# Performance work log

Hardware: AMD Instinct MI355X
Metric: run time of the kernel (lower is better)

## Reference

```python
import jax, jax.numpy as jnp
import numpy as np

N_Q = 9      # qubits -> state dim 512
N_L = 10     # circuit layers
DIM = 2 ** N_Q
B = 16384    # batch
N_CLS = 10


def _apply_1q(psi, U, q):
    # psi: [B, 2,...,2] (N_Q qubit axes); U: [2,2] complex
    psi = jnp.moveaxis(psi, q + 1, 1)
    shp = psi.shape
    psi = jnp.einsum('ij,bjk->bik', U, psi.reshape(shp[0], 2, -1)).reshape(shp)
    return jnp.moveaxis(psi, 1, q + 1)


def _apply_2q(psi, U, q0, q1):
    # U: [4,4] complex acting on (q0, q1)
    psi = jnp.moveaxis(psi, (q0 + 1, q1 + 1), (1, 2))
    shp = psi.shape
    psi = jnp.einsum('ij,bjk->bik', U, psi.reshape(shp[0], 4, -1)).reshape(shp)
    return jnp.moveaxis(psi, (1, 2), (q0 + 1, q1 + 1))


def _rot_mat(phi, theta, omega):
    # PennyLane Rot = RZ(omega) RY(theta) RZ(phi)
    c, s = jnp.cos(theta / 2), jnp.sin(theta / 2)
    a, b = (phi + omega) / 2, (phi - omega) / 2
    return jnp.stack([
        jnp.stack([jnp.exp(-1j * a) * c, -jnp.exp(1j * b) * s]),
        jnp.stack([jnp.exp(-1j * b) * s, jnp.exp(1j * a) * c]),
    ]).astype(jnp.complex64)


def _crx_mat(t):
    c, s = jnp.cos(t / 2), jnp.sin(t / 2)
    rx = jnp.stack([jnp.stack([c + 0j, -1j * s]),
                    jnp.stack([-1j * s, c + 0j])]).astype(jnp.complex64)
    return jnp.eye(4, dtype=jnp.complex64).at[2:, 2:].set(rx)


def _layer(psi, rot_n, crx_n):
    for i in range(N_Q):
        psi = _apply_1q(psi, _rot_mat(rot_n[i, 0], rot_n[i, 1], rot_n[i, 2]), i)
    for i in range(N_Q):
        psi = _apply_2q(psi, _crx_mat(crx_n[i, 0]), i, (i + 1) % N_Q)
    return psi


def _circuit(x, rot, crx):
    # AmplitudeEmbedding(normalize=True)
    psi = (x / jnp.linalg.norm(x, axis=1, keepdims=True)).astype(jnp.complex64)
    psi = psi.reshape((x.shape[0],) + (2,) * N_Q)
    for n in range(N_L):
        psi = _layer(psi, rot[n], crx[n])
    probs = psi.real ** 2 + psi.imag ** 2
    # <Z_q> = P(bit_q = 0) - P(bit_q = 1)
    zs = []
    for q in range(N_Q):
        axes = tuple(a for a in range(1, N_Q + 1) if a != q + 1)
        p = probs.sum(axis=axes)  # [B, 2]
        zs.append(p[:, 0] - p[:, 1])
    return jnp.stack(zs, axis=1)  # [B, N_Q]


def setup_inputs() -> dict:
    key = jax.random.key(0)
    k0, k1, k2, k3, k4 = jax.random.split(key, 5)
    x = jax.random.normal(k0, (B, DIM), jnp.float32)
    rot = jax.random.normal(k1, (N_L, N_Q, 3), jnp.float32)
    crx = jax.random.normal(k2, (N_L, N_Q, 1), jnp.float32)
    fc_w = jax.random.normal(k3, (N_CLS, N_Q), jnp.float32) * 0.3
    fc_b = jax.random.normal(k4, (N_CLS,), jnp.float32) * 0.1
    return {"x": x, "rot": rot, "crx": crx, "fc_w": fc_w, "fc_b": fc_b}


def reference(x, rot, crx, fc_w, fc_b):
    z = _circuit(x, rot, crx)          # [B, 9]
    logits = z @ fc_w.T + fc_b         # [B, 10]
    return jax.nn.log_softmax(logits, axis=1)
```

## Files before the change

kernel.cpp:

```cpp
#include <hip/hip_runtime.h>
#include <hip/hip_bf16.h>
#include <math.h>

#define NQ 9
#define NL 10
#define DIM 512
#define NCLS 10
#define B_TOT 16384

#define A_OFF   ((size_t)0)
#define BT_OFF  ((size_t)16 << 20)
#define ZP_OFF  ((size_t)32 << 20)
#define WS_NEED (((size_t)96) << 20)

__device__ __forceinline__ float shx(float v, int m) { return __shfl_xor(v, m, 64); }

__device__ __forceinline__ int looks_bf16(const void* p, int count) {
  const unsigned short* u = (const unsigned short*)p;
  int n = count < 64 ? count : 64;
  int good = 0;
  for (int i = 0; i < n; ++i) {
    unsigned short v = u[i];
    int e = (v >> 7) & 0xFF;
    good += (e >= 100 && e <= 140) || ((v & 0x7FFF) == 0);
  }
  return good * 8 >= n * 7;
}

__device__ __forceinline__ float ld(const void* p, int i, int isbf) {
  if (isbf) return __uint_as_float(((unsigned)((const unsigned short*)p)[i]) << 16);
  return ((const float*)p)[i];
}

template<int M>
__device__ __forceinline__ void rot_x(float (&sr)[8], float (&si)[8], const float* u) {
  float4 uA = *(const float4*)u;
  float4 uB = *(const float4*)(u + 4);
  bool hi = (threadIdx.x & M) != 0;
  float ar = hi ? uB.z : uA.x, ai = hi ? uB.w : uA.y;
  float br = hi ? uB.x : uA.z, bi = hi ? uB.y : uA.w;
#pragma unroll
  for (int r = 0; r < 8; ++r) {
    float pr = shx(sr[r], M), pi = shx(si[r], M);
    float nr = ar * sr[r] - ai * si[r] + br * pr - bi * pi;
    float ni = ar * si[r] + ai * sr[r] + br * pi + bi * pr;
    sr[r] = nr; si[r] = ni;
  }
}
template<int S>
__device__ __forceinline__ void rot_r(float (&sr)[8], float (&si)[8], const float* u) {
  float4 uA = *(const float4*)u;
  float4 uB = *(const float4*)(u + 4);
#pragma unroll
  for (int r0 = 0; r0 < 8; ++r0) {
    if (r0 & S) continue;
    int r1 = r0 + S;
    float a0r = sr[r0], a0i = si[r0], a1r = sr[r1], a1i = si[r1];
    sr[r0] = uA.x * a0r - uA.y * a0i + uA.z * a1r - uA.w * a1i;
    si[r0] = uA.x * a0i + uA.y * a0r + uA.z * a1i + uA.w * a1r;
    sr[r1] = uB.x * a0r - uB.y * a0i + uB.z * a1r - uB.w * a1i;
    si[r1] = uB.x * a0i + uB.y * a0r + uB.z * a1i + uB.w * a1r;
  }
}
template<int MC, int MT>
__device__ __forceinline__ void crx_ll(float (&sr)[8], float (&si)[8], const float* cs) {
  bool ctrl = (threadIdx.x & MC) != 0;
  float c = ctrl ? cs[0] : 1.0f;
  float s = ctrl ? cs[1] : 0.0f;
#pragma unroll
  for (int r = 0; r < 8; ++r) {
    float pr = shx(sr[r], MT), pi = shx(si[r], MT);
    float nr = c * sr[r] + s * pi;
    float ni = c * si[r] - s * pr;
    sr[r] = nr; si[r] = ni;
  }
}
template<int MC, int ST>
__device__ __forceinline__ void crx_lr(float (&sr)[8], float (&si)[8], const float* cs) {
  bool ctrl = (threadIdx.x & MC) != 0;
  float c = ctrl ? cs[0] : 1.0f;
  float s = ctrl ? cs[1] : 0.0f;
#pragma unroll
  for (int r0 = 0; r0 < 8; ++r0) {
    if (r0 & ST) continue;
    int r1 = r0 + ST;
    float a0r = sr[r0], a0i = si[r0], a1r = sr[r1], a1i = si[r1];
    sr[r0] = c * a0r + s * a1i;  si[r0] = c * a0i - s * a1r;
    sr[r1] = c * a1r + s * a0i;  si[r1] = c * a1i - s * a0r;
  }
}
template<int PC, int ST>
__device__ __forceinline__ void crx_rr(float (&sr)[8], float (&si)[8], const float* cs) {
  float c = cs[0], s = cs[1];
#pragma unroll
  for (int r0 = 0; r0 < 8; ++r0) {
    if (r0 & ST) continue;
    if (!((r0 >> PC) & 1)) continue;
    int r1 = r0 + ST;
    float a0r = sr[r0], a0i = si[r0], a1r = sr[r1], a1i = si[r1];
    sr[r0] = c * a0r + s * a1i;  si[r0] = c * a0i - s * a1r;
    sr[r1] = c * a1r + s * a0i;  si[r1] = c * a1i - s * a0r;
  }
}
template<int PC, int MT>
__device__ __forceinline__ void crx_rl(float (&sr)[8], float (&si)[8], const float* cs) {
  float c = cs[0], s = cs[1];
#pragma unroll
  for (int r = 0; r < 8; ++r) {
    if (!((r >> PC) & 1)) continue;
    float pr = shx(sr[r], MT), pi = shx(si[r], MT);
    float nr = c * sr[r] + s * pi;
    float ni = c * si[r] - s * pr;
    sr[r] = nr; si[r] = ni;
  }
}

__device__ __forceinline__ void build_gates(const void* rot, const void* crx,
                                            float* gU, float* gCS) {
  int tid = threadIdx.x;
  __shared__ int gflags[2];
  if (tid == 0) {
    gflags[0] = looks_bf16(rot, NL * NQ * 3);
    gflags[1] = looks_bf16(crx, NL * NQ);
  }
  __syncthreads();
  if (tid < NL * NQ) {
    int frot = gflags[0], fcrx = gflags[1];
    float phi = ld(rot, tid * 3 + 0, frot);
    float th  = ld(rot, tid * 3 + 1, frot);
    float om  = ld(rot, tid * 3 + 2, frot);
    float c = cosf(0.5f * th), s = sinf(0.5f * th);
    float a = 0.5f * (phi + om), b = 0.5f * (phi - om);
    float ca = cosf(a), sa = sinf(a), cb = cosf(b), sb = sinf(b);
    float* u = gU + tid * 8;
    u[0] =  ca * c; u[1] = -sa * c;
    u[2] = -cb * s; u[3] = -sb * s;
    u[4] =  cb * s; u[5] = -sb * s;
    u[6] =  ca * c; u[7] =  sa * c;
    float t2 = 0.5f * ld(crx, tid, fcrx);
    gCS[tid * 2 + 0] = cosf(t2);
    gCS[tid * 2 + 1] = sinf(t2);
  }
  __syncthreads();
}

__device__ __forceinline__ void run_circuit(float (&sr)[8], float (&si)[8],
                                            const float* gU, const float* gCS) {
#pragma unroll 1
  for (int n = 0; n < NL; ++n) {
    const float* U  = gU  + n * NQ * 8;
    const float* CS = gCS + n * NQ * 2;
    rot_x<32>(sr, si, U + 0 * 8);
    rot_x<16>(sr, si, U + 1 * 8);
    rot_x< 8>(sr, si, U + 2 * 8);
    rot_x< 4>(sr, si, U + 3 * 8);
    rot_x< 2>(sr, si, U + 4 * 8);
    rot_x< 1>(sr, si, U + 5 * 8);
    rot_r< 4>(sr, si, U + 6 * 8);
    rot_r< 2>(sr, si, U + 7 * 8);
    rot_r< 1>(sr, si, U + 8 * 8);
    crx_ll<32, 16>(sr, si, CS + 0 * 2);
    crx_ll<16,  8>(sr, si, CS + 1 * 2);
    crx_ll< 8,  4>(sr, si, CS + 2 * 2);
    crx_ll< 4,  2>(sr, si, CS + 3 * 2);
    crx_ll< 2,  1>(sr, si, CS + 4 * 2);
    crx_lr< 1,  4>(sr, si, CS + 5 * 2);
    crx_rr< 2,  2>(sr, si, CS + 6 * 2);
    crx_rr< 1,  1>(sr, si, CS + 7 * 2);
    crx_rl< 0, 32>(sr, si, CS + 8 * 2);
  }
}

template<int M>
__device__ __forceinline__ void rot_lane2(float (&sr)[2], float (&si)[2], const float* u) {
  float4 uA = *(const float4*)u;
  float4 uB = *(const float4*)(u + 4);
  bool hi = (threadIdx.x & M) != 0;
  float ar = hi ? uB.z : uA.x, ai = hi ? uB.w : uA.y;
  float br = hi ? uB.x : uA.z, bi = hi ? uB.y : uA.w;
#pragma unroll
  for (int r = 0; r < 2; ++r) {
    float pr = shx(sr[r], M), pi = shx(si[r], M);
    float nr = ar * sr[r] - ai * si[r] + br * pr - bi * pi;
    float ni = ar * si[r] + ai * sr[r] + br * pi + bi * pr;
    sr[r] = nr; si[r] = ni;
  }
}
__device__ __forceinline__ void rot_reg2(float (&sr)[2], float (&si)[2], const float* u) {
  float4 uA = *(const float4*)u;
  float4 uB = *(const float4*)(u + 4);
  float a0r = sr[0], a0i = si[0], a1r = sr[1], a1i = si[1];
  sr[0] = uA.x * a0r - uA.y * a0i + uA.z * a1r - uA.w * a1i;
  si[0] = uA.x * a0i + uA.y * a0r + uA.z * a1i + uA.w * a1r;
  sr[1] = uB.x * a0r - uB.y * a0i + uB.z * a1r - uB.w * a1i;
  si[1] = uB.x * a0i + uB.y * a0r + uB.z * a1i + uB.w * a1r;
}
__device__ __forceinline__ void crx_lane2(float (&sr)[2], float (&si)[2],
                                          float c, float s, int MT) {
#pragma unroll
  for (int r = 0; r < 2; ++r) {
    float pr = shx(sr[r], MT), pi = shx(si[r], MT);
    float nr = c * sr[r] + s * pi;
    float ni = c * si[r] - s * pr;
    sr[r] = nr; si[r] = ni;
  }
}
__device__ __forceinline__ void crx_reg2(float (&sr)[2], float (&si)[2], float c, float s) {
  float a0r = sr[0], a0i = si[0], a1r = sr[1], a1i = si[1];
  sr[0] = c * a0r + s * a1i;  si[0] = c * a0i - s * a1r;
  sr[1] = c * a1r + s * a0i;  si[1] = c * a1i - s * a0r;
}

__global__ __launch_bounds__(256) void prep_kernel(const void* __restrict__ x,
                                                   const void* __restrict__ rot,
                                                   const void* __restrict__ crx,
                                                   __hip_bfloat16* __restrict__ A,
                                                   __hip_bfloat16* __restrict__ BT) {
  int tid = threadIdx.x;
  if (blockIdx.x < DIM) {
    __shared__ __align__(16) float gU[NL * NQ * 8];
    __shared__ __align__(16) float gCS[NL * NQ * 2];
    __shared__ float sRe[DIM], sIm[DIM];
    build_gates(rot, crx, gU, gCS);
    int lane = tid & 63, wv = tid >> 6;
    int idx0 = wv * 128 + lane * 2;
    int k = blockIdx.x;
    float sr[2], si[2];
    sr[0] = (idx0 == k) ? 1.f : 0.f;
    sr[1] = (idx0 + 1 == k) ? 1.f : 0.f;
    si[0] = si[1] = 0.f;
#pragma unroll 1
    for (int n = 0; n < NL; ++n) {
      const float* U   = gU  + n * NQ * 8;
      const float* CS  = gCS + n * NQ * 2;
      const float* CSp = gCS + (n - 1) * NQ * 2;
      __syncthreads();
      sRe[idx0] = sr[0]; sIm[idx0] = si[0];
      sRe[idx0 + 1] = sr[1]; sIm[idx0 + 1] = si[1];
      __syncthreads();
      {
        const float* U0 = U; const float* U1 = U + 8;
        int a = wv >> 1, b = wv & 1;
        float mr[4], mi[4];
#pragma unroll
        for (int w2 = 0; w2 < 4; ++w2) {
          int a2 = w2 >> 1, b2 = w2 & 1;
          float u0r = U0[(a * 2 + a2) * 2], u0i = U0[(a * 2 + a2) * 2 + 1];
          float u1r = U1[(b * 2 + b2) * 2], u1i = U1[(b * 2 + b2) * 2 + 1];
          mr[w2] = u0r * u1r - u0i * u1i;
          mi[w2] = u0r * u1i + u0i * u1r;
        }
        float x0r[4], x0i[4], v1r[4], v1i[4];
#pragma unroll
        for (int w2 = 0; w2 < 4; ++w2) {
          x0r[w2] = sRe[w2 * 128 + lane * 2 + 0];
          x0i[w2] = sIm[w2 * 128 + lane * 2 + 0];
          v1r[w2] = sRe[w2 * 128 + lane * 2 + 1];
          v1i[w2] = sIm[w2 * 128 + lane * 2 + 1];
        }
        float x1r[4], x1i[4];
        if (n > 0) {
          float cp = CSp[16], sp = CSp[17];
#pragma unroll
          for (int w2 = 0; w2 < 4; ++w2) {
            x1r[w2] = cp * v1r[w2] + sp * v1i[w2 ^ 2];
            x1i[w2] = cp * v1i[w2] - sp * v1r[w2 ^ 2];
          }
        } else {
#pragma unroll
          for (int w2 = 0; w2 < 4; ++w2) { x1r[w2] = v1r[w2]; x1i[w2] = v1i[w2]; }
        }
        float nr0 = 0.f, ni0 = 0.f, nr1 = 0.f, ni1 = 0.f;
#pragma unroll
        for (int w2 = 0; w2 < 4; ++w2) {
          nr0 += mr[w2] * x0r[w2] - mi[w2] * x0i[w2];
          ni0 += mr[w2] * x0i[w2] + mi[w2] * x0r[w2];
          nr1 += mr[w2] * x1r[w2] - mi[w2] * x1i[w2];
          ni1 += mr[w2] * x1i[w2] + mi[w2] * x1r[w2];
        }
        sr[0] = nr0; si[0] = ni0; sr[1] = nr1; si[1] = ni1;
      }
      rot_lane2<32>(sr, si, U + 2 * 8);
      rot_lane2<16>(sr, si, U + 3 * 8);
      rot_lane2< 8>(sr, si, U + 4 * 8);
      rot_lane2< 4>(sr, si, U + 5 * 8);
      rot_lane2< 2>(sr, si, U + 6 * 8);
      rot_lane2< 1>(sr, si, U + 7 * 8);
      rot_reg2(sr, si, U + 8 * 8);
      __syncthreads();
      sRe[idx0] = sr[0]; sIm[idx0] = si[0];
      sRe[idx0 + 1] = sr[1]; sIm[idx0 + 1] = si[1];
      __syncthreads();
      {
        float c = (wv & 2) ? CS[0] : 1.f, s = (wv & 2) ? CS[1] : 0.f;
        int p0 = (wv ^ 1) * 128 + lane * 2;
#pragma unroll
        for (int r = 0; r < 2; ++r) {
          float pr = sRe[p0 + r], pi = sIm[p0 + r];
          float nr = c * sr[r] + s * pi;
          float ni = c * si[r] - s * pr;
          sr[r] = nr; si[r] = ni;
        }
      }
      { float c = (wv & 1) ? CS[2] : 1.f, s = (wv & 1) ? CS[3] : 0.f;
        crx_lane2(sr, si, c, s, 32); }
      { bool ct = (lane & 32); crx_lane2(sr, si, ct ? CS[4] : 1.f, ct ? CS[5] : 0.f, 16); }
      { bool ct = (lane & 16); crx_lane2(sr, si, ct ? CS[6] : 1.f, ct ? CS[7] : 0.f, 8); }
      { bool ct = (lane &  8); crx_lane2(sr, si, ct ? CS[8] : 1.f, ct ? CS[9] : 0.f, 4); }
      { bool ct = (lane &  4); crx_lane2(sr, si, ct ? CS[10] : 1.f, ct ? CS[11] : 0.f, 2); }
      { bool ct = (lane &  2); crx_lane2(sr, si, ct ? CS[12] : 1.f, ct ? CS[13] : 0.f, 1); }
      { bool ct = (lane & 1); crx_reg2(sr, si, ct ? CS[14] : 1.f, ct ? CS[15] : 0.f); }
    }
    __syncthreads();
    sRe[idx0] = sr[0]; sIm[idx0] = si[0];
    sRe[idx0 + 1] = sr[1]; sIm[idx0 + 1] = si[1];
    __syncthreads();
    {
      const float* CS9 = gCS + (NL - 1) * NQ * 2;
      float c = CS9[16], s = CS9[17];
      int p1 = (wv ^ 2) * 128 + lane * 2 + 1;
      float pr = sRe[p1], pi = sIm[p1];
      float nr = c * sr[1] + s * pi;
      float ni = c * si[1] - s * pr;
      sr[1] = nr; si[1] = ni;
    }
#pragma unroll
    for (int r = 0; r < 2; ++r) {
      int j = idx0 + r;
      BT[(size_t)j * DIM + k]         = __float2bfloat16(sr[r]);
      BT[(size_t)(DIM + j) * DIM + k] = __float2bfloat16(si[r]);
    }
  } else {
    __shared__ int fx;
    if (tid == 0) fx = looks_bf16(x, B_TOT * DIM);
    __syncthreads();
    size_t i0 = ((size_t)(blockIdx.x - DIM) * 256 + tid) * 8;
    if (fx) {
      *(uint4*)(A + i0) = *(const uint4*)((const unsigned short*)x + i0);
    } else {
      const float4* src = (const float4*)((const float*)x + i0);
      float4 a = src[0], b = src[1];
      __hip_bfloat16 o[8];
      o[0] = __float2bfloat16(a.x); o[1] = __float2bfloat16(a.y);
      o[2] = __float2bfloat16(a.z); o[3] = __float2bfloat16(a.w);
      o[4] = __float2bfloat16(b.x); o[5] = __float2bfloat16(b.y);
      o[6] = __float2bfloat16(b.z); o[7] = __float2bfloat16(b.w);
      *(uint4*)(A + i0) = *(uint4*)o;
    }
  }
}

using frag8 = __attribute__((ext_vector_type(8))) short;
using frag4 = __attribute__((ext_vector_type(4))) float;

typedef __attribute__((address_space(1))) const unsigned int GU32;
typedef __attribute__((address_space(3))) unsigned int LU32;
__device__ __forceinline__ void async16(const void* g, void* l) {
  __builtin_amdgcn_global_load_lds((GU32*)g, (LU32*)l, 16, 0, 0);
}

#define VM(N) asm volatile("s_waitcnt vmcnt(" #N ")" ::: "memory")
#define BARR  do { __builtin_amdgcn_sched_barrier(0); \
                   __builtin_amdgcn_s_barrier(); \
                   __builtin_amdgcn_sched_barrier(0); } while (0)

#define STG_A(NB, T1, H) do { \
  async16(gA + ((size_t)((H) * 128) * 512 + (T1) * 64),     dA + (NB) * 16384 + (H) * 8192); \
  async16(gA + ((size_t)((H) * 128 + 8) * 512 + (T1) * 64), dA + (NB) * 16384 + (H) * 8192 + 512); \
} while (0)
#define STG_B(NB, T1, H) do { \
  async16(gB + ((size_t)((H) * 128) * 512 + (T1) * 64),     dB + (NB) * 16384 + (H) * 8192); \
  async16(gB + ((size_t)((H) * 128 + 8) * 512 + (T1) * 64), dB + (NB) * 16384 + (H) * 8192 + 512); \
} while (0)

#define PHASE(CURB, QM, QN, STG, VMC) do { \
  frag8 paf[4][2], pbf[2][2]; \
  _Pragma("unroll") \
  for (int mi = 0; mi < 4; ++mi) { \
    _Pragma("unroll") \
    for (int kk = 0; kk < 2; ++kk) \
      paf[mi][kk] = *(const frag8*)(lsm + (CURB) * 16384 + \
        ((QM) * 128 + wm * 64 + mi * 16 + r15) * 64 + \
        (((kk * 4 + quad) ^ (r15 & 7)) * 8)); \
  } \
  _Pragma("unroll") \
  for (int ni = 0; ni < 2; ++ni) { \
    _Pragma("unroll") \
    for (int kk = 0; kk < 2; ++kk) \
      pbf[ni][kk] = *(const frag8*)(lsm + 32768 + (CURB) * 16384 + \
        ((QN) * 128 + wn * 32 + ni * 16 + r15) * 64 + \
        (((kk * 4 + quad) ^ (r15 & 7)) * 8)); \
  } \
  STG; \
  __builtin_amdgcn_s_setprio(1); \
  _Pragma("unroll") \
  for (int mi = 0; mi < 4; ++mi) { \
    _Pragma("unroll") \
    for (int ni = 0; ni < 2; ++ni) { \
      acc[QM][mi][QN][ni] = __builtin_amdgcn_mfma_f32_16x16x32_bf16( \
          paf[mi][0], pbf[ni][0], acc[QM][mi][QN][ni], 0, 0, 0); \
      acc[QM][mi][QN][ni] = __builtin_amdgcn_mfma_f32_16x16x32_bf16( \
          paf[mi][1], pbf[ni][1], acc[QM][mi][QN][ni], 0, 0, 0); \
    } \
  } \
  __builtin_amdgcn_s_setprio(0); \
  VMC; \
} while (0)

__global__ __launch_bounds__(512, 2) void gemm_z_kernel(const unsigned short* __restrict__ A,
                                                        const unsigned short* __restrict__ BT,
                                                        float* __restrict__ Zp) {
  __shared__ __align__(16) unsigned short lsm[65536];
  int bid = blockIdx.x;
  int xcd = bid & 7;
  int ii = bid >> 3;
  int m0 = (xcd * 8 + (ii >> 2)) * 256;
  int n0 = (ii & 3) * 256;
  int tid = threadIdx.x;
  int wv = tid >> 6, lane = tid & 63;
  int wm = wv >> 2, wn = wv & 3;
  int r15 = lane & 15, quad = lane >> 4;
  int lr3 = lane >> 3;
  int scol = ((lane & 7) ^ lr3) * 8;
  const unsigned short* gA = A + (size_t)(m0 + wv * 16 + lr3) * 512 + scol;
  const unsigned short* gB = BT + (size_t)(n0 + wv * 16 + lr3) * 512 + scol;
  unsigned short* dA = lsm + wv * 16 * 64;
  unsigned short* dB = lsm + 32768 + wv * 16 * 64;

  frag4 acc[2][4][2][2] = {};

  STG_A(0, 0, 0); STG_B(0, 0, 0); STG_A(0, 0, 1); STG_B(0, 0, 1);
  VM(4);
  BARR;

#pragma unroll 1
  for (int t = 0; t < 7; ++t) {
    const int cur = t & 1, nb = cur ^ 1;
    PHASE(cur, 0, 0, STG_A(nb, t + 1, 0), VM(4)); BARR;
    PHASE(cur, 1, 0, STG_B(nb, t + 1, 0), VM(4)); BARR;
    PHASE(cur, 0, 1, STG_A(nb, t + 1, 1), ;);
    PHASE(cur, 1, 1, STG_B(nb, t + 1, 1), VM(4)); BARR;
  }
  PHASE(1, 0, 0, ;, VM(2)); BARR;
  PHASE(1, 1, 0, ;, VM(0)); BARR;
  PHASE(1, 0, 1, ;, ;);
  PHASE(1, 1, 1, ;, ;);
  __syncthreads();

#pragma unroll
  for (int qm = 0; qm < 2; ++qm)
#pragma unroll
    for (int mi = 0; mi < 4; ++mi)
#pragma unroll
      for (int qn = 0; qn < 2; ++qn)
#pragma unroll
        for (int ni = 0; ni < 2; ++ni)
#pragma unroll
          for (int rg = 0; rg < 4; ++rg) {
            float v = acc[qm][mi][qn][ni][rg];
            float p = v * v;
            int prow = qm * 128 + wm * 64 + mi * 16 + quad * 4 + rg;
            int pcol = qn * 128 + wn * 32 + ni * 16 + r15;
            int phys = (pcol >> 3) ^ (prow & 7);
            __hip_bfloat16 h = __float2bfloat16(p);
            lsm[prow * 256 + phys * 8 + (pcol & 7)] = *(unsigned short*)&h;
          }
  __syncthreads();

  frag8 b2[8];
#pragma unroll
  for (int kk = 0; kk < 8; ++kk) {
    union { frag8 f; unsigned short u[8]; } bb;
#pragma unroll
    for (int e = 0; e < 8; ++e) {
      int j = (n0 + kk * 32 + quad * 8 + e) & 511;
      unsigned short us;
      if (r15 < 9)      us = ((((unsigned)j) >> ((8 - r15) & 31)) & 1) ? 0xBF80 : 0x3F80;
      else if (r15 == 9) us = 0x3F80;
      else               us = 0;
      bb.u[e] = us;
    }
    b2[kk] = bb.f;
  }
  frag4 z2[2] = {};
#pragma unroll
  for (int tt = 0; tt < 2; ++tt) {
    int mt = wv + tt * 8;
#pragma unroll
    for (int kk = 0; kk < 8; ++kk) {
      frag8 a2 = *(const frag8*)(lsm + (mt * 16 + r15) * 256 +
                                 (((kk * 4 + quad) ^ (r15 & 7)) * 8));
      z2[tt] = __builtin_amdgcn_mfma_f32_16x16x32_bf16(a2, b2[kk], z2[tt], 0, 0, 0);
    }
  }
  int panel = n0 >> 8;
  if (r15 < 10) {
#pragma unroll
    for (int tt = 0; tt < 2; ++tt) {
      int mt = wv + tt * 8;
#pragma unroll
      for (int rg = 0; rg < 4; ++rg) {
        int mrow = m0 + mt * 16 + quad * 4 + rg;
        Zp[(size_t)panel * (B_TOT * 10) + (size_t)mrow * 10 + r15] = z2[tt][rg];
      }
    }
  }
}

__global__ __launch_bounds__(128) void zred_kernel(const float* __restrict__ Zp,
                                                   const void* __restrict__ fcw,
                                                   const void* __restrict__ fcb,
                                                   float* __restrict__ out) {
  __shared__ int flags[2];
  __shared__ float sW[NCLS * NQ];
  __shared__ float sB[NCLS];
  int tid = threadIdx.x;
  if (tid == 0) {
    flags[0] = looks_bf16(fcw, NCLS * NQ);
    flags[1] = looks_bf16(fcb, NCLS);
  }
  __syncthreads();
  if (tid < NCLS * NQ) sW[tid] = ld(fcw, tid, flags[0]);
  if (tid < NCLS)      sB[tid] = ld(fcb, tid, flags[1]);
  __syncthreads();
  int row = blockIdx.x * 128 + tid;
  float z[10];
#pragma unroll
  for (int q = 0; q < 10; ++q) z[q] = 0.f;
#pragma unroll
  for (int pnl = 0; pnl < 4; ++pnl) {
    const float* p = Zp + (size_t)pnl * (B_TOT * 10) + (size_t)row * 10;
#pragma unroll
    for (int q = 0; q < 10; ++q) z[q] += p[q];
  }
  float invP = 1.0f / z[9];
#pragma unroll
  for (int q = 0; q < NQ; ++q) z[q] *= invP;
  float lg[NCLS], mx = -1e30f;
#pragma unroll
  for (int k = 0; k < NCLS; ++k) {
    float t = sB[k];
#pragma unroll
    for (int q = 0; q < NQ; ++q) t += z[q] * sW[k * NQ + q];
    lg[k] = t; mx = fmaxf(mx, t);
  }
  float se = 0.f;
#pragma unroll
  for (int k = 0; k < NCLS; ++k) se += expf(lg[k] - mx);
  float lse = mx + logf(se);
#pragma unroll
  for (int k = 0; k < NCLS; ++k) out[(size_t)row * NCLS + k] = lg[k] - lse;
}

__global__ __launch_bounds__(256) void qnn_kernel(
    const void* __restrict__ x, const void* __restrict__ rot,
    const void* __restrict__ crx, const void* __restrict__ fcw,
    const void* __restrict__ fcb, float* __restrict__ out) {
  __shared__ __align__(16) float gU[NL * NQ * 8];
  __shared__ __align__(16) float gCS[NL * NQ * 2];
  __shared__ int flags[3];
  int tid = threadIdx.x;
  if (tid == 0) {
    flags[0] = looks_bf16(x, B_TOT * DIM);
    flags[1] = looks_bf16(fcw, NCLS * NQ);
    flags[2] = looks_bf16(fcb, NCLS);
  }
  build_gates(rot, crx, gU, gCS);
  __syncthreads();
  int wid = (blockIdx.x * blockDim.x + tid) >> 6;
  int lane = tid & 63;
  float sr[8], si[8];
  if (flags[0]) {
    const uint4 u = *(const uint4*)((const unsigned short*)x + (size_t)wid * DIM + lane * 8);
    sr[0] = __uint_as_float(u.x << 16); sr[1] = __uint_as_float(u.x & 0xffff0000u);
    sr[2] = __uint_as_float(u.y << 16); sr[3] = __uint_as_float(u.y & 0xffff0000u);
    sr[4] = __uint_as_float(u.z << 16); sr[5] = __uint_as_float(u.z & 0xffff0000u);
    sr[6] = __uint_as_float(u.w << 16); sr[7] = __uint_as_float(u.w & 0xffff0000u);
  } else {
    const float4* xf = (const float4*)((const float*)x + (size_t)wid * DIM) + lane * 2;
    float4 a = xf[0], b = xf[1];
    sr[0] = a.x; sr[1] = a.y; sr[2] = a.z; sr[3] = a.w;
    sr[4] = b.x; sr[5] = b.y; sr[6] = b.z; sr[7] = b.w;
  }
  float nrm = 0.f;
#pragma unroll
  for (int r = 0; r < 8; ++r) { nrm += sr[r] * sr[r]; si[r] = 0.f; }
#pragma unroll
  for (int m = 1; m < 64; m <<= 1) nrm += shx(nrm, m);
  float inv = rsqrtf(nrm);
  inv = inv * (1.5f - 0.5f * nrm * inv * inv);
#pragma unroll
  for (int r = 0; r < 8; ++r) sr[r] *= inv;
  run_circuit(sr, si, gU, gCS);
  float p[8], P = 0.f;
#pragma unroll
  for (int r = 0; r < 8; ++r) { p[r] = sr[r] * sr[r] + si[r] * si[r]; P += p[r]; }
  float z[NQ];
#pragma unroll
  for (int q = 0; q < 6; ++q) z[q] = (lane & (32 >> q)) ? -P : P;
  z[6] = z[7] = z[8] = 0.f;
#pragma unroll
  for (int r = 0; r < 8; ++r) {
    z[6] += (r & 4) ? -p[r] : p[r];
    z[7] += (r & 2) ? -p[r] : p[r];
    z[8] += (r & 1) ? -p[r] : p[r];
  }
#pragma unroll
  for (int m = 1; m < 64; m <<= 1) {
#pragma unroll
    for (int q = 0; q < NQ; ++q) z[q] += shx(z[q], m);
  }
  int ffw = flags[1], ffb = flags[2];
  float lg[NCLS], mx = -1e30f;
#pragma unroll
  for (int k = 0; k < NCLS; ++k) {
    float t = ld(fcb, k, ffb);
#pragma unroll
    for (int q = 0; q < NQ; ++q) t += z[q] * ld(fcw, k * NQ + q, ffw);
    lg[k] = t; mx = fmaxf(mx, t);
  }
  float se = 0.f;
#pragma unroll
  for (int k = 0; k < NCLS; ++k) se += expf(lg[k] - mx);
  float lse = mx + logf(se);
  if (lane < NCLS) out[(size_t)wid * NCLS + lane] = lg[lane] - lse;
}

extern "C" void kernel_launch(void* const* d_in, const int* in_sizes, int n_in,
                              void* d_out, int out_size, void* d_ws, size_t ws_size,
                              hipStream_t stream) {
  const void* x   = d_in[0];
  const void* rot = d_in[1];
  const void* crx = d_in[2];
  const void* fcw = d_in[3];
  const void* fcb = d_in[4];
  float* out = (float*)d_out;
  if (ws_size >= WS_NEED) {
    __hip_bfloat16* A  = (__hip_bfloat16*)((char*)d_ws + A_OFF);
    __hip_bfloat16* BT = (__hip_bfloat16*)((char*)d_ws + BT_OFF);
    float*          Zp = (float*)((char*)d_ws + ZP_OFF);
    prep_kernel<<<DIM + (B_TOT * DIM) / (256 * 8), 256, 0, stream>>>(x, rot, crx, A, BT);
    gemm_z_kernel<<<(B_TOT / 256) * (1024 / 256), 512, 0, stream>>>(
        (const unsigned short*)A, (const unsigned short*)BT, Zp);
    zred_kernel<<<B_TOT / 128, 128, 0, stream>>>(Zp, fcw, fcb, out);
  } else {
    qnn_kernel<<<(B_TOT * 64) / 256, 256, 0, stream>>>(x, rot, crx, fcw, fcb, out);
  }
}
```

Baseline: 135.8 us.

## Build circuit unitary columns one per wavefront via run_circuit

Changes how the prep kernel builds the circuit's unitary columns. Before, each 256-thread block simulated one basis column, using shared memory and block barriers for the cross-wave qubits. Now each wavefront simulates one column with 8 amplitudes per lane, using the existing run_circuit shuffle/register path, so there is no LDS traffic or __syncthreads. This cuts the prep blocks from 512 to 128, in exchange for more registers per thread and 4x fewer waves doing the gate simulation.

```diff
diff --git a/kernel.cpp b/kernel.cpp
--- a/kernel.cpp
+++ b/kernel.cpp
@@ -171,45 +171,7 @@
   }
 }
 
-template<int M>
-__device__ __forceinline__ void rot_lane2(float (&sr)[2], float (&si)[2], const float* u) {
-  float4 uA = *(const float4*)u;
-  float4 uB = *(const float4*)(u + 4);
-  bool hi = (threadIdx.x & M) != 0;
-  float ar = hi ? uB.z : uA.x, ai = hi ? uB.w : uA.y;
-  float br = hi ? uB.x : uA.z, bi = hi ? uB.y : uA.w;
-#pragma unroll
-  for (int r = 0; r < 2; ++r) {
-    float pr = shx(sr[r], M), pi = shx(si[r], M);
-    float nr = ar * sr[r] - ai * si[r] + br * pr - bi * pi;
-    float ni = ar * si[r] + ai * sr[r] + br * pi + bi * pr;
-    sr[r] = nr; si[r] = ni;
-  }
-}
-__device__ __forceinline__ void rot_reg2(float (&sr)[2], float (&si)[2], const float* u) {
-  float4 uA = *(const float4*)u;
-  float4 uB = *(const float4*)(u + 4);
-  float a0r = sr[0], a0i = si[0], a1r = sr[1], a1i = si[1];
-  sr[0] = uA.x * a0r - uA.y * a0i + uA.z * a1r - uA.w * a1i;
-  si[0] = uA.x * a0i + uA.y * a0r + uA.z * a1i + uA.w * a1r;
-  sr[1] = uB.x * a0r - uB.y * a0i + uB.z * a1r - uB.w * a1i;
-  si[1] = uB.x * a0i + uB.y * a0r + uB.z * a1i + uB.w * a1r;
-}
-__device__ __forceinline__ void crx_lane2(float (&sr)[2], float (&si)[2],
-                                          float c, float s, int MT) {
-#pragma unroll
-  for (int r = 0; r < 2; ++r) {
-    float pr = shx(sr[r], MT), pi = shx(si[r], MT);
-    float nr = c * sr[r] + s * pi;
-    float ni = c * si[r] - s * pr;
-    sr[r] = nr; si[r] = ni;
-  }
-}
-__device__ __forceinline__ void crx_reg2(float (&sr)[2], float (&si)[2], float c, float s) {
-  float a0r = sr[0], a0i = si[0], a1r = sr[1], a1i = si[1];
-  sr[0] = c * a0r + s * a1i;  si[0] = c * a0i - s * a1r;
-  sr[1] = c * a1r + s * a0i;  si[1] = c * a1i - s * a0r;
-}
+#define WB (DIM / 4)
 
 __global__ __launch_bounds__(256) void prep_kernel(const void* __restrict__ x,
                                                    const void* __restrict__ rot,
@@ -217,116 +179,22 @@
                                                    __hip_bfloat16* __restrict__ A,
                                                    __hip_bfloat16* __restrict__ BT) {
   int tid = threadIdx.x;
-  if (blockIdx.x < DIM) {
+  if (blockIdx.x < WB) {
     __shared__ __align__(16) float gU[NL * NQ * 8];
     __shared__ __align__(16) float gCS[NL * NQ * 2];
-    __shared__ float sRe[DIM], sIm[DIM];
     build_gates(rot, crx, gU, gCS);
     int lane = tid & 63, wv = tid >> 6;
-    int idx0 = wv * 128 + lane * 2;
-    int k = blockIdx.x;
-    float sr[2], si[2];
-    sr[0] = (idx0 == k) ? 1.f : 0.f;
-    sr[1] = (idx0 + 1 == k) ? 1.f : 0.f;
-    si[0] = si[1] = 0.f;
-#pragma unroll 1
-    for (int n = 0; n < NL; ++n) {
-      const float* U   = gU  + n * NQ * 8;
-      const float* CS  = gCS + n * NQ * 2;
-      const float* CSp = gCS + (n - 1) * NQ * 2;
-      __syncthreads();
-      sRe[idx0] = sr[0]; sIm[idx0] = si[0];
-      sRe[idx0 + 1] = sr[1]; sIm[idx0 + 1] = si[1];
-      __syncthreads();
-      {
-        const float* U0 = U; const float* U1 = U + 8;
-        int a = wv >> 1, b = wv & 1;
-        float mr[4], mi[4];
-#pragma unroll
-        for (int w2 = 0; w2 < 4; ++w2) {
-          int a2 = w2 >> 1, b2 = w2 & 1;
-          float u0r = U0[(a * 2 + a2) * 2], u0i = U0[(a * 2 + a2) * 2 + 1];
-          float u1r = U1[(b * 2 + b2) * 2], u1i = U1[(b * 2 + b2) * 2 + 1];
-          mr[w2] = u0r * u1r - u0i * u1i;
-          mi[w2] = u0r * u1i + u0i * u1r;
-        }
-        float x0r[4], x0i[4], v1r[4], v1i[4];
-#pragma unroll
-        for (int w2 = 0; w2 < 4; ++w2) {
-          x0r[w2] = sRe[w2 * 128 + lane * 2 + 0];
-          x0i[w2] = sIm[w2 * 128 + lane * 2 + 0];
-          v1r[w2] = sRe[w2 * 128 + lane * 2 + 1];
-          v1i[w2] = sIm[w2 * 128 + lane * 2 + 1];
-        }
-        float x1r[4], x1i[4];
-        if (n > 0) {
-          float cp = CSp[16], sp = CSp[17];
-#pragma unroll
-          for (int w2 = 0; w2 < 4; ++w2) {
-            x1r[w2] = cp * v1r[w2] + sp * v1i[w2 ^ 2];
-            x1i[w2] = cp * v1i[w2] - sp * v1r[w2 ^ 2];
-          }
-        } else {
-#pragma unroll
-          for (int w2 = 0; w2 < 4; ++w2) { x1r[w2] = v1r[w2]; x1i[w2] = v1i[w2]; }
-        }
-        float nr0 = 0.f, ni0 = 0.f, nr1 = 0.f, ni1 = 0.f;
-#pragma unroll
-        for (int w2 = 0; w2 < 4; ++w2) {
-          nr0 += mr[w2] * x0r[w2] - mi[w2] * x0i[w2];
-          ni0 += mr[w2] * x0i[w2] + mi[w2] * x0r[w2];
-          nr1 += mr[w2] * x1r[w2] - mi[w2] * x1i[w2];
-          ni1 += mr[w2] * x1i[w2] + mi[w2] * x1r[w2];
-        }
-        sr[0] = nr0; si[0] = ni0; sr[1] = nr1; si[1] = ni1;
-      }
-      rot_lane2<32>(sr, si, U + 2 * 8);
-      rot_lane2<16>(sr, si, U + 3 * 8);
-      rot_lane2< 8>(sr, si, U + 4 * 8);
-      rot_lane2< 4>(sr, si, U + 5 * 8);
-      rot_lane2< 2>(sr, si, U + 6 * 8);
-      rot_lane2< 1>(sr, si, U + 7 * 8);
-      rot_reg2(sr, si, U + 8 * 8);
-      __syncthreads();
-      sRe[idx0] = sr[0]; sIm[idx0] = si[0];
-      sRe[idx0 + 1] = sr[1]; sIm[idx0 + 1] = si[1];
-      __syncthreads();
-      {
-        float c = (wv & 2) ? CS[0] : 1.f, s = (wv & 2) ? CS[1] : 0.f;
-        int p0 = (wv ^ 1) * 128 + lane * 2;
-#pragma unroll
-        for (int r = 0; r < 2; ++r) {
-          float pr = sRe[p0 + r], pi = sIm[p0 + r];
-          float nr = c * sr[r] + s * pi;
-          float ni = c * si[r] - s * pr;
-          sr[r] = nr; si[r] = ni;
-        }
-      }
-      { float c = (wv & 1) ? CS[2] : 1.f, s = (wv & 1) ? CS[3] : 0.f;
-        crx_lane2(sr, si, c, s, 32); }
-      { bool ct = (lane & 32); crx_lane2(sr, si, ct ? CS[4] : 1.f, ct ? CS[5] : 0.f, 16); }
-      { bool ct = (lane & 16); crx_lane2(sr, si, ct ? CS[6] : 1.f, ct ? CS[7] : 0.f, 8); }
-      { bool ct = (lane &  8); crx_lane2(sr, si, ct ? CS[8] : 1.f, ct ? CS[9] : 0.f, 4); }
-      { bool ct = (lane &  4); crx_lane2(sr, si, ct ? CS[10] : 1.f, ct ? CS[11] : 0.f, 2); }
-      { bool ct = (lane &  2); crx_lane2(sr, si, ct ? CS[12] : 1.f, ct ? CS[13] : 0.f, 1); }
-      { bool ct = (lane & 1); crx_reg2(sr, si, ct ? CS[14] : 1.f, ct ? CS[15] : 0.f); }
+    int k = blockIdx.x * 4 + wv;
+    float sr[8], si[8];
+#pragma unroll
+    for (int r = 0; r < 8; ++r) {
+      sr[r] = (lane * 8 + r == k) ? 1.f : 0.f;
+      si[r] = 0.f;
     }
-    __syncthreads();
-    sRe[idx0] = sr[0]; sIm[idx0] = si[0];
-    sRe[idx0 + 1] = sr[1]; sIm[idx0 + 1] = si[1];
-    __syncthreads();
-    {
-      const float* CS9 = gCS + (NL - 1) * NQ * 2;
-      float c = CS9[16], s = CS9[17];
-      int p1 = (wv ^ 2) * 128 + lane * 2 + 1;
-      float pr = sRe[p1], pi = sIm[p1];
-      float nr = c * sr[1] + s * pi;
-      float ni = c * si[1] - s * pr;
-      sr[1] = nr; si[1] = ni;
-    }
-#pragma unroll
-    for (int r = 0; r < 2; ++r) {
-      int j = idx0 + r;
+    run_circuit(sr, si, gU, gCS);
+#pragma unroll
+    for (int r = 0; r < 8; ++r) {
+      int j = lane * 8 + r;
       BT[(size_t)j * DIM + k]         = __float2bfloat16(sr[r]);
       BT[(size_t)(DIM + j) * DIM + k] = __float2bfloat16(si[r]);
     }
@@ -334,7 +202,7 @@
     __shared__ int fx;
     if (tid == 0) fx = looks_bf16(x, B_TOT * DIM);
     __syncthreads();
-    size_t i0 = ((size_t)(blockIdx.x - DIM) * 256 + tid) * 8;
+    size_t i0 = ((size_t)(blockIdx.x - WB) * 256 + tid) * 8;
     if (fx) {
       *(uint4*)(A + i0) = *(const uint4*)((const unsigned short*)x + i0);
     } else {
@@ -639,7 +507,7 @@
     __hip_bfloat16* A  = (__hip_bfloat16*)((char*)d_ws + A_OFF);
     __hip_bfloat16* BT = (__hip_bfloat16*)((char*)d_ws + BT_OFF);
     float*          Zp = (float*)((char*)d_ws + ZP_OFF);
-    prep_kernel<<<DIM + (B_TOT * DIM) / (256 * 8), 256, 0, stream>>>(x, rot, crx, A, BT);
+    prep_kernel<<<WB + (B_TOT * DIM) / (256 * 8), 256, 0, stream>>>(x, rot, crx, A, BT);
     gemm_z_kernel<<<(B_TOT / 256) * (1024 / 256), 512, 0, stream>>>(
         (const unsigned short*)A, (const unsigned short*)BT, Zp);
     zred_kernel<<<B_TOT / 128, 128, 0, stream>>>(Zp, fcw, fcb, out);
```

New measurement: 148.9 us. 1.1x slower.
